# Performance work log

Measured on AMD Instinct MI355X. Metric: run time of the kernel, lower is better.

The kernel has to match this reference:

```python
import jax, jax.numpy as jnp
import numpy as np

B, S, D = 8, 4096, 768
HEADS = 12
NEIGHBORS = 2
DILATION = 1
KERNEL = 1 + 2 * NEIGHBORS  # 5
DIM_HEAD = D // HEADS


def setup_inputs() -> dict:
    key = jax.random.key(0)
    ks = jax.random.split(key, 11)
    sc = 1.0 / np.sqrt(D)
    return {
        "x": jax.random.normal(ks[0], (B, S, D), dtype=jnp.float32),
        "Wq": jax.random.normal(ks[1], (D, D), dtype=jnp.float32) * sc,
        "bq": jax.random.normal(ks[2], (D,), dtype=jnp.float32) * 0.02,
        "Wk": jax.random.normal(ks[3], (D, D), dtype=jnp.float32) * sc,
        "bk": jax.random.normal(ks[4], (D,), dtype=jnp.float32) * 0.02,
        "Wv": jax.random.normal(ks[5], (D, D), dtype=jnp.float32) * sc,
        "bv": jax.random.normal(ks[6], (D,), dtype=jnp.float32) * 0.02,
        "Wo": jax.random.normal(ks[7], (D, D), dtype=jnp.float32) * sc,
        "bo": jax.random.normal(ks[8], (D,), dtype=jnp.float32) * 0.02,
        "gamma": jnp.ones((D,), dtype=jnp.float32),
        "beta": jnp.zeros((D,), dtype=jnp.float32),
    }


def _extract_seq_patches(x, kernel_size, dilation):
    # [B, S, D] -> [B, S, kernel_size, D] of dilated local windows, zero-padded.
    seq_len = x.shape[1]
    patch_size = kernel_size + (dilation - 1) * (kernel_size - 1)
    pad_r = (patch_size - 1) // 2
    pad_l = patch_size - pad_r - 1
    xp = jnp.pad(x, ((0, 0), (pad_l, pad_r), (0, 0)))
    # small fixed loop over kernel positions (kernel_size = 5)
    return jnp.stack([xp[:, i:i + seq_len] for i in range(0, patch_size, dilation)], axis=2)


def reference(x, Wq, bq, Wk, bk, Wv, bv, Wo, bo, gamma, beta):
    patches = _extract_seq_patches(x, KERNEL, DILATION)  # [B, S, K, D]
    q = x @ Wq + bq                                       # [B, S, D]
    k = patches @ Wk + bk                                 # [B, S, K, D]
    v = patches @ Wv + bv                                 # [B, S, K, D]
    # split heads
    q = q.reshape(B, S, HEADS, DIM_HEAD)
    k = k.reshape(B, S, KERNEL, HEADS, DIM_HEAD)
    v = v.reshape(B, S, KERNEL, HEADS, DIM_HEAD)
    scale = jnp.sqrt(jnp.asarray(DIM_HEAD, dtype=q.dtype))
    scores = jnp.einsum('bshd,bskhd->bshk', q, k) / scale  # [B, S, H, K]
    p = jax.nn.softmax(scores, axis=-1)
    att = jnp.einsum('bshk,bskhd->bshd', p, v)             # [B, S, H, dh]
    att = att.reshape(B, S, D)
    att = att @ Wo + bo
    y = att + x
    # LayerNorm over last dim
    mu = jnp.mean(y, axis=-1, keepdims=True)
    var = jnp.var(y, axis=-1, keepdims=True)
    y = (y - mu) / jnp.sqrt(var + 1e-5) * gamma + beta
    return y
```

## Files before the change

kernel.cpp:

```cpp
#include <hip/hip_runtime.h>

#define B_  8
#define S_  4096
#define D_  768
#define H_  12
#define M_  (B_ * S_)
#define NQKV_ 2304
#define NTILES 12

typedef unsigned short u16;
typedef __attribute__((ext_vector_type(4))) float  f32x4;
typedef __attribute__((ext_vector_type(8))) __bf16 bf16x8;
typedef __attribute__((ext_vector_type(4))) u16    u16x4;

#define GAS __attribute__((address_space(1)))
#define LAS __attribute__((address_space(3)))

__device__ __forceinline__ u16 f2bf(float f) {
    unsigned u = __float_as_uint(f);
    u += 0x7FFF + ((u >> 16) & 1);
    return (u16)(u >> 16);
}
__device__ __forceinline__ float bf2f(u16 h) {
    return __uint_as_float(((unsigned)h) << 16);
}

__device__ __forceinline__ void gload_lds16(const void* g, void* l) {
    __builtin_amdgcn_global_load_lds((const GAS void*)g, (LAS void*)l, 16, 0, 0);
}

__device__ __forceinline__ int xcd_swz(int bid, int nwg) {
    return (bid & 7) * (nwg >> 3) + (bid >> 3);
}

__global__ __launch_bounds__(256) void castx_kernel(const float* __restrict__ x,
                                                    u16* __restrict__ xb) {
    const int i = blockIdx.x * 256 + threadIdx.x;
    const float4 v = ((const float4*)x)[i];
    u16x4 o;
    o.x = f2bf(v.x); o.y = f2bf(v.y); o.z = f2bf(v.z); o.w = f2bf(v.w);
    ((u16x4*)xb)[i] = o;
}

__global__ __launch_bounds__(256) void wtrans_kernel(const float* __restrict__ Wq,
                                                     const float* __restrict__ Wk,
                                                     const float* __restrict__ Wv,
                                                     const float* __restrict__ Wo,
                                                     u16* __restrict__ Wb) {
    const float* W = (blockIdx.z == 0) ? Wq : (blockIdx.z == 1) ? Wk
                   : (blockIdx.z == 2) ? Wv : Wo;
    u16* O = Wb + (size_t)blockIdx.z * D_ * D_;
    __shared__ float tile[32][33];
    const int tx = threadIdx.x & 31, ty = threadIdx.x >> 5;
    const int k0 = blockIdx.y * 32, n0 = blockIdx.x * 32;
#pragma unroll
    for (int j = 0; j < 4; j++)
        tile[ty + j * 8][tx] = W[(size_t)(k0 + ty + j * 8) * D_ + n0 + tx];
    __syncthreads();
#pragma unroll
    for (int j = 0; j < 4; j++)
        O[(size_t)(n0 + ty + j * 8) * D_ + k0 + tx] = f2bf(tile[tx][ty + j * 8]);
}


#define BAR()                                                \
    __builtin_amdgcn_sched_barrier(0);                       \
    __builtin_amdgcn_s_barrier();                            \
    __builtin_amdgcn_sched_barrier(0)

#define VMBAR(N)                                             \
    __builtin_amdgcn_sched_barrier(0);                       \
    asm volatile("s_waitcnt vmcnt(" #N ")" ::: "memory");    \
    __builtin_amdgcn_s_barrier();                            \
    __builtin_amdgcn_sched_barrier(0)

#define MFMA_Q(AF, BF, MO, NO)                                               \
    __builtin_amdgcn_s_setprio(1);                                           \
    _Pragma("unroll") for (int mi = 0; mi < 4; ++mi)                         \
        _Pragma("unroll") for (int ni = 0; ni < 2; ++ni)                     \
            _Pragma("unroll") for (int kh = 0; kh < 2; ++kh)                 \
                acc[mi + MO][ni + NO] =                                      \
                    __builtin_amdgcn_mfma_f32_16x16x32_bf16(                 \
                        AF[mi][kh], BF[ni][kh], acc[mi + MO][ni + NO], 0, 0, 0); \
    __builtin_amdgcn_s_setprio(0)

#define RD(p, imm) (*(const bf16x8*)((p) + (imm)))

template <int MODE>
__global__ __launch_bounds__(512, 2) void gemm8_kernel(
    const u16* __restrict__ A, const u16* __restrict__ Wb,
    const float* __restrict__ b0, const float* __restrict__ b1,
    const float* __restrict__ b2,
    u16* __restrict__ outb, const u16* __restrict__ xres) {
    extern __shared__ char lds[];

    const int t = threadIdx.x;
    const int w = t >> 6, l = t & 63;
    const int wm = w >> 2, wn = w & 3;

    const int NTN = (MODE == 0) ? 9 : 3;
    const int work = xcd_swz(blockIdx.x, gridDim.x);
    const int mt = work / NTN, nt = work % NTN;
    const int m0 = mt * 256;
    const int n0 = nt * 256;
    const int widx = (MODE == 0) ? (n0 / D_) : 3;
    const int n0w = n0 - ((MODE == 0) ? widx * D_ : 0);

    const int srow   = t >> 3;
    const int schunk = (t & 7) ^ (srow & 7);
    const u16* Asrc = A + (size_t)(m0 + srow) * D_ + schunk * 8;
    const u16* Bsrc = Wb + (size_t)widx * (D_ * D_) + (size_t)(n0w + srow) * D_ + schunk * 8;

    auto STAGE_A = [&](int h, int tk, int db) {
        const u16* s = Asrc + (size_t)(h * 128) * D_ + tk * 64;
        char* d = lds + db * 65536 + h * 16384 + (w << 10);
        gload_lds16(s, d);
        gload_lds16(s + 64 * D_, d + 8192);
    };
    auto STAGE_B = [&](int h, int tk, int db) {
        const u16* s = Bsrc + (size_t)(h * 128) * D_ + tk * 64;
        char* d = lds + db * 65536 + 32768 + h * 16384 + (w << 10);
        gload_lds16(s, d);
        gload_lds16(s + 64 * D_, d + 8192);
    };

    const int ck0 = (((l >> 4) ^ (l & 7)) << 4);
    const int ck1 = ((((l >> 4) + 4) ^ (l & 7)) << 4);
    const int aRowB = (wm * 128 + (l & 15)) * 128;
    const int bRowB = 32768 + (wn * 64 + (l & 15)) * 128;
    const char* aC0[2] = { lds + aRowB + ck0, lds + 65536 + aRowB + ck0 };
    const char* aC1[2] = { lds + aRowB + ck1, lds + 65536 + aRowB + ck1 };
    const char* bC0[2] = { lds + bRowB + ck0, lds + 65536 + bRowB + ck0 };
    const char* bC1[2] = { lds + bRowB + ck1, lds + 65536 + bRowB + ck1 };

    f32x4 acc[8][4];
#pragma unroll
    for (int i = 0; i < 8; i++)
#pragma unroll
        for (int j = 0; j < 4; j++) acc[i][j] = (f32x4){0.f, 0.f, 0.f, 0.f};

    bf16x8 Alo[4][2], Ahi[4][2], Ba[2][2], Bb[2][2];

    STAGE_A(0, 0, 0); STAGE_A(1, 0, 0); STAGE_B(0, 0, 0); STAGE_B(1, 0, 0);
    STAGE_B(1, 1, 1); STAGE_A(0, 1, 1); STAGE_A(1, 1, 1);
    __builtin_amdgcn_sched_barrier(0);
    asm volatile("s_waitcnt vmcnt(6)" ::: "memory");
    __builtin_amdgcn_s_barrier();
    __builtin_amdgcn_sched_barrier(0);
#pragma unroll
    for (int mi = 0; mi < 4; ++mi) {
        Alo[mi][0] = RD(aC0[0], mi * 2048);
        Alo[mi][1] = RD(aC1[0], mi * 2048);
    }
#pragma unroll
    for (int ni = 0; ni < 2; ++ni) {
        Ba[ni][0] = RD(bC0[0], ni * 2048);
        Ba[ni][1] = RD(bC1[0], ni * 2048);
    }

#pragma unroll
    for (int X = 0; X < NTILES; ++X) {
        const int c = X & 1;
        const int o = c ^ 1;
        const int t1 = (X + 1 < NTILES) ? X + 1 : X + 1 - NTILES;
        const int t2 = (X + 2 < NTILES) ? X + 2 : X + 2 - NTILES;

#pragma unroll
        for (int ni = 0; ni < 2; ++ni) {
            Bb[ni][0] = RD(bC0[c], (ni + 2) * 2048);
            Bb[ni][1] = RD(bC1[c], (ni + 2) * 2048);
        }
#pragma unroll
        for (int mi = 0; mi < 4; ++mi) {
            Ahi[mi][0] = RD(aC0[c], (mi + 4) * 2048);
            Ahi[mi][1] = RD(aC1[c], (mi + 4) * 2048);
        }
        STAGE_B(0, t1, o);
        MFMA_Q(Alo, Ba, 0, 0);
        BAR();

        STAGE_B(1, t2, c);
        MFMA_Q(Alo, Bb, 0, 2);
        VMBAR(4);

        if (X + 1 < NTILES) {
#pragma unroll
            for (int mi = 0; mi < 4; ++mi) {
                Alo[mi][0] = RD(aC0[o], mi * 2048);
                Alo[mi][1] = RD(aC1[o], mi * 2048);
            }
        }
        STAGE_A(0, t2, c);
        MFMA_Q(Ahi, Ba, 4, 0);
        VMBAR(4);

        if (X + 1 < NTILES) {
#pragma unroll
            for (int ni = 0; ni < 2; ++ni) {
                Ba[ni][0] = RD(bC0[o], ni * 2048);
                Ba[ni][1] = RD(bC1[o], ni * 2048);
            }
        }
        STAGE_A(1, t2, c);
        MFMA_Q(Ahi, Bb, 4, 2);
        BAR();
    }

    const int crow0 = m0 + wm * 128 + ((l >> 4) << 2);
    const int ccol0 = n0 + wn * 64 + (l & 15);
    if (MODE == 0) {
        const float* bias = (widx == 0) ? b0 : (widx == 1) ? b1 : b2;
        const int bcol0 = ccol0 - widx * D_;
#pragma unroll
        for (int mi = 0; mi < 8; ++mi)
#pragma unroll
            for (int ni = 0; ni < 4; ++ni) {
                const float bv = bias[bcol0 + ni * 16];
#pragma unroll
                for (int r = 0; r < 4; ++r)
                    outb[(size_t)(crow0 + mi * 16 + r) * NQKV_ + ccol0 + ni * 16] =
                        f2bf(acc[mi][ni][r] + bv);
            }
    } else {
#pragma unroll
        for (int mi = 0; mi < 8; ++mi)
#pragma unroll
            for (int ni = 0; ni < 4; ++ni) {
                const int col = ccol0 + ni * 16;
                const float bv = b0[col];
#pragma unroll
                for (int r = 0; r < 4; ++r) {
                    const size_t idx = (size_t)(crow0 + mi * 16 + r) * D_ + col;
                    outb[idx] = f2bf(acc[mi][ni][r] + bv + bf2f(xres[idx]));
                }
            }
    }
}

__global__ __launch_bounds__(256) void attn_kernel(const u16* __restrict__ QKV,
                                                   const float* __restrict__ bk,
                                                   const float* __restrict__ bv,
                                                   u16* __restrict__ att) {
    const int gw = xcd_swz(blockIdx.x, gridDim.x) * 4 + (threadIdx.x >> 6);
    const int l  = threadIdx.x & 63;
    const int hq = gw % 3;
    const int m  = gw / 3;
    const int s  = m & (S_ - 1);
    const int col = hq * 256 + l * 4;
    const u16* base = QKV + (size_t)m * NQKV_;

    const u16x4 qv = *(const u16x4*)(base + col);
    float qf[4];
#pragma unroll
    for (int j = 0; j < 4; j++) qf[j] = bf2f(qv[j]);

    float sc[5];
#pragma unroll
    for (int i = 0; i < 5; i++) {
        const int sp = s + i - 2;
        float p;
        if (sp >= 0 && sp < S_) {
            const u16x4 kv = *(const u16x4*)(base + (i - 2) * NQKV_ + D_ + col);
            p = qf[0] * bf2f(kv[0]) + qf[1] * bf2f(kv[1])
              + qf[2] * bf2f(kv[2]) + qf[3] * bf2f(kv[3]);
        } else {
            const float4 kb = *(const float4*)(bk + col);
            p = qf[0] * kb.x + qf[1] * kb.y + qf[2] * kb.z + qf[3] * kb.w;
        }
#pragma unroll
        for (int off = 1; off < 16; off <<= 1) p += __shfl_xor(p, off, 64);
        sc[i] = p * 0.125f;
    }
    float mx = sc[0];
#pragma unroll
    for (int i = 1; i < 5; i++) mx = fmaxf(mx, sc[i]);
    float e[5], sum = 0.f;
#pragma unroll
    for (int i = 0; i < 5; i++) { e[i] = __expf(sc[i] - mx); sum += e[i]; }
    const float inv = 1.f / sum;

    float o[4] = {0.f, 0.f, 0.f, 0.f};
#pragma unroll
    for (int i = 0; i < 5; i++) {
        const float wgt = e[i] * inv;
        const int sp = s + i - 2;
        if (sp >= 0 && sp < S_) {
            const u16x4 vv = *(const u16x4*)(base + (i - 2) * NQKV_ + 2 * D_ + col);
#pragma unroll
            for (int j = 0; j < 4; j++) o[j] += wgt * bf2f(vv[j]);
        } else {
            const float4 vb = *(const float4*)(bv + col);
            o[0] += wgt * vb.x; o[1] += wgt * vb.y;
            o[2] += wgt * vb.z; o[3] += wgt * vb.w;
        }
    }
    u16x4 ov;
#pragma unroll
    for (int j = 0; j < 4; j++) ov[j] = f2bf(o[j]);
    *(u16x4*)(att + (size_t)m * D_ + col) = ov;
}

__global__ __launch_bounds__(256) void ln_kernel(const u16* __restrict__ Yb,
                                                 const float* __restrict__ gamma,
                                                 const float* __restrict__ beta,
                                                 float* __restrict__ out) {
    const int row = blockIdx.x;
    const u16* r = Yb + (size_t)row * D_;
    const int t = threadIdx.x;
    const float v0 = bf2f(r[t]), v1 = bf2f(r[t + 256]), v2 = bf2f(r[t + 512]);
    float s  = v0 + v1 + v2;
    float s2 = v0 * v0 + v1 * v1 + v2 * v2;
#pragma unroll
    for (int off = 32; off > 0; off >>= 1) {
        s  += __shfl_xor(s,  off, 64);
        s2 += __shfl_xor(s2, off, 64);
    }
    __shared__ float red[8];
    const int w = t >> 6, l = t & 63;
    if (l == 0) { red[w] = s; red[4 + w] = s2; }
    __syncthreads();
    s  = red[0] + red[1] + red[2] + red[3];
    s2 = red[4] + red[5] + red[6] + red[7];
    const float mu  = s * (1.f / 768.f);
    const float var = s2 * (1.f / 768.f) - mu * mu;
    const float inv = rsqrtf(var + 1e-5f);
    float* o = out + (size_t)row * D_;
    o[t]       = (v0 - mu) * inv * gamma[t]       + beta[t];
    o[t + 256] = (v1 - mu) * inv * gamma[t + 256] + beta[t + 256];
    o[t + 512] = (v2 - mu) * inv * gamma[t + 512] + beta[t + 512];
}

extern "C" void kernel_launch(void* const* d_in, const int* in_sizes, int n_in,
                              void* d_out, int out_size, void* d_ws, size_t ws_size,
                              hipStream_t stream) {
    const float* x     = (const float*)d_in[0];
    const float* Wq    = (const float*)d_in[1];
    const float* bq    = (const float*)d_in[2];
    const float* Wk    = (const float*)d_in[3];
    const float* bk    = (const float*)d_in[4];
    const float* Wv    = (const float*)d_in[5];
    const float* bv    = (const float*)d_in[6];
    const float* Wo    = (const float*)d_in[7];
    const float* bo    = (const float*)d_in[8];
    const float* gamma = (const float*)d_in[9];
    const float* beta  = (const float*)d_in[10];

    char* ws = (char*)d_ws;
    u16*   Wb  = (u16*)ws;
    u16*   xb  = (u16*)(ws + 4718592);
    u16*   QKV = (u16*)(ws + 4718592 + 50331648);
    u16*   yb  = QKV;
    u16*   att = (u16*)d_out;

    (void)hipFuncSetAttribute(reinterpret_cast<const void*>(&gemm8_kernel<0>),
                              hipFuncAttributeMaxDynamicSharedMemorySize, 131072);
    (void)hipFuncSetAttribute(reinterpret_cast<const void*>(&gemm8_kernel<1>),
                              hipFuncAttributeMaxDynamicSharedMemorySize, 131072);

    castx_kernel<<<(M_ * D_) / (256 * 4), 256, 0, stream>>>(x, xb);
    wtrans_kernel<<<dim3(24, 24, 4), 256, 0, stream>>>(Wq, Wk, Wv, Wo, Wb);
    gemm8_kernel<0><<<(M_ / 256) * 9, 512, 131072, stream>>>(xb, Wb, bq, bk, bv,
                                                             QKV, nullptr);
    attn_kernel<<<(M_ * 3) / 4, 256, 0, stream>>>(QKV, bk, bv, att);
    gemm8_kernel<1><<<(M_ / 256) * 3, 512, 131072, stream>>>(att, Wb, bo, nullptr, nullptr,
                                                             yb, xb);
    ln_kernel<<<M_, 256, 0, stream>>>(yb, gamma, beta, (float*)d_out);
}
```

Baseline: 327.3 us.

## Restructure GEMM main loop into ping-pong phases with barriers around MFMA clusters

Reorganizes the pipelined bf16 GEMM main loop so each of the four phases loads its LDS fragments, issues one global-to-LDS stage, then brackets its MFMA cluster with a barrier-in (waiting on LDS reads) and a barrier-out. The prologue now prefetches B for tile 1 instead of A, and the A/B staging order and distances change. The intent is a cleaner two-wave ping-pong schedule where memory phases of one wave overlap MFMA phases of another. It adds more barriers per iteration and lgkmcnt waits, which may expose latency if the waves do not interleave as planned.

```diff
diff --git a/kernel.cpp b/kernel.cpp
--- a/kernel.cpp
+++ b/kernel.cpp
@@ -63,12 +63,18 @@
 }
 
 
-#define BAR()                                                \
+#define PH_IN()                                              \
+    __builtin_amdgcn_sched_barrier(0);                       \
+    __builtin_amdgcn_s_barrier();                            \
+    asm volatile("s_waitcnt lgkmcnt(0)" ::: "memory");       \
+    __builtin_amdgcn_sched_barrier(0)
+
+#define PH_OUT()                                             \
     __builtin_amdgcn_sched_barrier(0);                       \
     __builtin_amdgcn_s_barrier();                            \
     __builtin_amdgcn_sched_barrier(0)
 
-#define VMBAR(N)                                             \
+#define PH_OUT_VM(N)                                         \
     __builtin_amdgcn_sched_barrier(0);                       \
     asm volatile("s_waitcnt vmcnt(" #N ")" ::: "memory");    \
     __builtin_amdgcn_s_barrier();                            \
@@ -142,21 +148,11 @@
     bf16x8 Alo[4][2], Ahi[4][2], Ba[2][2], Bb[2][2];
 
     STAGE_A(0, 0, 0); STAGE_A(1, 0, 0); STAGE_B(0, 0, 0); STAGE_B(1, 0, 0);
-    STAGE_B(1, 1, 1); STAGE_A(0, 1, 1); STAGE_A(1, 1, 1);
+    STAGE_B(0, 1, 1); STAGE_B(1, 1, 1);
     __builtin_amdgcn_sched_barrier(0);
-    asm volatile("s_waitcnt vmcnt(6)" ::: "memory");
+    asm volatile("s_waitcnt vmcnt(4)" ::: "memory");
     __builtin_amdgcn_s_barrier();
     __builtin_amdgcn_sched_barrier(0);
-#pragma unroll
-    for (int mi = 0; mi < 4; ++mi) {
-        Alo[mi][0] = RD(aC0[0], mi * 2048);
-        Alo[mi][1] = RD(aC1[0], mi * 2048);
-    }
-#pragma unroll
-    for (int ni = 0; ni < 2; ++ni) {
-        Ba[ni][0] = RD(bC0[0], ni * 2048);
-        Ba[ni][1] = RD(bC1[0], ni * 2048);
-    }
 
 #pragma unroll
     for (int X = 0; X < NTILES; ++X) {
@@ -166,45 +162,48 @@
         const int t2 = (X + 2 < NTILES) ? X + 2 : X + 2 - NTILES;
 
 #pragma unroll
+        for (int mi = 0; mi < 4; ++mi) {
+            Alo[mi][0] = RD(aC0[c], mi * 2048);
+            Alo[mi][1] = RD(aC1[c], mi * 2048);
+        }
+#pragma unroll
+        for (int ni = 0; ni < 2; ++ni) {
+            Ba[ni][0] = RD(bC0[c], ni * 2048);
+            Ba[ni][1] = RD(bC1[c], ni * 2048);
+        }
+        STAGE_A(0, t1, o);
+        asm volatile("s_waitcnt lgkmcnt(8)" ::: "memory");
+        PH_IN();
+        MFMA_Q(Alo, Ba, 0, 0);
+        PH_OUT();
+
+#pragma unroll
         for (int ni = 0; ni < 2; ++ni) {
             Bb[ni][0] = RD(bC0[c], (ni + 2) * 2048);
             Bb[ni][1] = RD(bC1[c], (ni + 2) * 2048);
         }
+        STAGE_A(1, t1, o);
+        PH_IN();
+        MFMA_Q(Alo, Bb, 0, 2);
+        PH_OUT();
+
 #pragma unroll
         for (int mi = 0; mi < 4; ++mi) {
             Ahi[mi][0] = RD(aC0[c], (mi + 4) * 2048);
             Ahi[mi][1] = RD(aC1[c], (mi + 4) * 2048);
         }
-        STAGE_B(0, t1, o);
-        MFMA_Q(Alo, Ba, 0, 0);
-        BAR();
+        STAGE_B(0, t2, c);
+        PH_IN();
+        MFMA_Q(Ahi, Ba, 4, 0);
+        PH_OUT();
 
         STAGE_B(1, t2, c);
-        MFMA_Q(Alo, Bb, 0, 2);
-        VMBAR(4);
-
-        if (X + 1 < NTILES) {
-#pragma unroll
-            for (int mi = 0; mi < 4; ++mi) {
-                Alo[mi][0] = RD(aC0[o], mi * 2048);
-                Alo[mi][1] = RD(aC1[o], mi * 2048);
-            }
-        }
-        STAGE_A(0, t2, c);
-        MFMA_Q(Ahi, Ba, 4, 0);
-        VMBAR(4);
-
-        if (X + 1 < NTILES) {
-#pragma unroll
-            for (int ni = 0; ni < 2; ++ni) {
-                Ba[ni][0] = RD(bC0[o], ni * 2048);
-                Ba[ni][1] = RD(bC1[o], ni * 2048);
-            }
-        }
-        STAGE_A(1, t2, c);
+        PH_IN();
         MFMA_Q(Ahi, Bb, 4, 2);
-        BAR();
-    }
+        PH_OUT_VM(4);
+    }
+
+    asm volatile("s_waitcnt vmcnt(0)" ::: "memory");
 
     const int crow0 = m0 + wm * 128 + ((l >> 4) << 2);
     const int ccol0 = n0 + wn * 64 + (l & 15);
```

After: 300.9 us. -8.1%, faster.
